# Performance work log

Measured on AMD Instinct MI355X. Metric: run time of the kernel, lower is better.

## Reference

```python
import jax, jax.numpy as jnp
import numpy as np

N, E, IN, HID, OUT, L = 50000, 800000, 128, 64, 40, 3


def setup_inputs() -> dict:
    key = jax.random.key(0)
    ks = jax.random.split(key, 10)
    x = jax.random.normal(ks[0], (N, IN), jnp.float32)
    edge_index = jax.random.randint(ks[1], (2, E), 0, N, dtype=jnp.int32)

    def u(k, shape, fan_in):
        s = 1.0 / np.sqrt(fan_in)
        return jax.random.uniform(k, shape, jnp.float32, -s, s)

    return {
        "x": x,
        "edge_index": edge_index,
        # former1 (NWGformerF): in -> hidden projection
        "Wf": u(ks[2], (IN, HID), IN),
        "bf": jnp.zeros((HID,), jnp.float32),
        # stacked GCNConv weights (hidden->hidden)
        "conv_W": u(ks[3], (L, HID, HID), HID),
        "conv_b": jnp.zeros((L, HID), jnp.float32),
        # residual linears
        "lin_W": u(ks[4], (L, HID, HID), HID),
        "lin_b": u(ks[5], (L, HID), HID),
        # batchnorm (eval mode: affine with running stats)
        "gamma": jnp.ones((L, HID), jnp.float32),
        "beta": jnp.zeros((L, HID), jnp.float32),
        "run_mean": jnp.zeros((L, HID), jnp.float32),
        "run_var": jnp.ones((L, HID), jnp.float32),
        # output head
        "pred_W": u(ks[6], (HID, OUT), HID),
        "pred_b": jnp.zeros((OUT,), jnp.float32),
    }


def reference(x, edge_index, Wf, bf, conv_W, conv_b, lin_W, lin_b,
              gamma, beta, run_mean, run_var, pred_W, pred_b):
    n = x.shape[0]
    src, dst = edge_index[0], edge_index[1]
    eps = 1e-5

    # GCN symmetric normalization with self-loops: deg over dst (+1 self loop)
    deg = jax.ops.segment_sum(jnp.ones(src.shape[0], x.dtype), dst,
                              num_segments=n) + 1.0
    dinv = jax.lax.rsqrt(deg)                      # [N]
    edge_coef = dinv[src] * dinv[dst]              # [E]
    self_coef = (dinv * dinv)[:, None]             # [N,1]

    def gcn(h, W, b):
        hw = h @ W                                 # [N,HID]
        agg = jax.ops.segment_sum(hw[src] * edge_coef[:, None], dst,
                                  num_segments=n)
        return agg + hw * self_coef + b

    # former1: in -> hidden (dropout is identity in eval mode)
    h = x @ Wf + bf

    for i in range(L):
        h = gcn(h, conv_W[i], conv_b[i]) + h @ lin_W[i] + lin_b[i]  # res
        h = (h - run_mean[i]) * (gamma[i] * jax.lax.rsqrt(run_var[i] + eps)) + beta[i]
        h = jax.nn.relu(h)

    return h @ pred_W + pred_b
```

## Files before the change

### kernel.cpp

```cpp
#include <hip/hip_runtime.h>
#include <hip/hip_bf16.h>
#include <hip/hip_fp16.h>

#define IN_DIM 128
#define HID 64
#define OUT_DIM 40
#define SPAD 68
#define CHUNKS 128

typedef __hip_bfloat16 bf16;
typedef unsigned short u16;
typedef _Float16 f16;
typedef __attribute__((ext_vector_type(8))) _Float16 f16x8;
typedef __attribute__((ext_vector_type(4))) float f32x4;

__device__ __forceinline__ float b2f(bf16 v) { return __bfloat162float(v); }
__device__ __forceinline__ float relu_f(float x) { return 0.5f * (x + fabsf(x)); }
__device__ __forceinline__ float ldv(const void* p, int i, int is32) {
    return is32 ? ((const float*)p)[i] : b2f(((const bf16*)p)[i]);
}

__global__ void MPNNs_60198261620971_kernel() {}

__global__ void canary_k(float* out, int m) {
    int i = blockIdx.x * blockDim.x + threadIdx.x;
    if (i < m) out[i] = 1234.0f;
}


__global__ __launch_bounds__(256) void hist_k(const int* __restrict__ dst,
                                              unsigned int* __restrict__ cnt,
                                              u16* __restrict__ rank,
                                              int e, int n, int n2, int chunk,
                                              const unsigned int* __restrict__ rv,
                                              int* __restrict__ flag) {
    __shared__ unsigned int hc[16384];
    if (blockIdx.x == 0 && threadIdx.x == 0)
        flag[0] = (rv[0] == 0x3F800000u) ? 1 : 0;
    int c = blockIdx.x >> 1, hf = blockIdx.x & 1;
    int w0 = hf << 14;
    int w1 = min(n2, w0 + 16384);
    int nw = w1 - w0;
    if (nw <= 0) return;
    for (int i = threadIdx.x; i < nw; i += 256) hc[i] = 0;
    __syncthreads();
    int e0 = c * chunk, e1 = min(e, e0 + chunk);
    for (int i = e0 + threadIdx.x; i < e1; i += 256) {
        int d = dst[i];
        if ((unsigned)d < (unsigned)n) {
            int w = d >> 1;
            if (w >= w0 && w < w1) {
                int sh = (d & 1) * 16;
                unsigned old = atomicAdd(&hc[w - w0], 1u << sh);
                rank[i] = (u16)((old >> sh) & 0xFFFFu);
            }
        }
    }
    __syncthreads();
    for (int i = threadIdx.x; i < nw; i += 256)
        cnt[(size_t)c * n2 + w0 + i] = hc[i];
}

__global__ __launch_bounds__(256) void former_k(const void* __restrict__ x,
                                                const void* __restrict__ Wf,
                                                const void* __restrict__ bfv,
                                                const int* __restrict__ dflag,
                                                float* __restrict__ h, int n) {
    __shared__ __align__(16) f16 wT[HID][IN_DIM + 8];
    int is32 = dflag[0];
    for (int i = threadIdx.x; i < IN_DIM * HID; i += 256) {
        int k = i >> 6, nn = i & 63;
        wT[nn][k] = (f16)ldv(Wf, i, is32);
    }
    __syncthreads();
    int wave = threadIdx.x >> 6, lane = threadIdx.x & 63;
    int m = lane & 15, quad = lane >> 4;
    int row0 = blockIdx.x * 64 + wave * 16;
    if (row0 >= n) return;
    int ar = row0 + m;
    int arc = (ar < n) ? ar : (n - 1);
    f16x8 a[4];
    if (is32) {
        const float* xp = (const float*)x + (size_t)arc * IN_DIM;
        #pragma unroll
        for (int cn = 0; cn < 4; cn++) {
            float4 u0 = *(const float4*)(xp + cn * 32 + quad * 8);
            float4 u1 = *(const float4*)(xp + cn * 32 + quad * 8 + 4);
            a[cn] = (f16x8){ (f16)u0.x, (f16)u0.y, (f16)u0.z, (f16)u0.w,
                             (f16)u1.x, (f16)u1.y, (f16)u1.z, (f16)u1.w };
        }
    } else {
        const bf16* xp = (const bf16*)x + (size_t)arc * IN_DIM;
        #pragma unroll
        for (int cn = 0; cn < 4; cn++)
            #pragma unroll
            for (int j = 0; j < 8; j++) a[cn][j] = (f16)b2f(xp[cn * 32 + quad * 8 + j]);
    }
    f32x4 acc[4];
    #pragma unroll
    for (int ct = 0; ct < 4; ct++) acc[ct] = (f32x4){0.f, 0.f, 0.f, 0.f};
    #pragma unroll
    for (int ct = 0; ct < 4; ct++) {
        int nn = ct * 16 + m;
        #pragma unroll
        for (int cn = 0; cn < 4; cn++) {
            f16x8 b = *(const f16x8*)&wT[nn][cn * 32 + quad * 8];
            acc[ct] = __builtin_amdgcn_mfma_f32_16x16x32_f16(a[cn], b, acc[ct], 0, 0, 0);
        }
    }
    float bias[4];
    #pragma unroll
    for (int ct = 0; ct < 4; ct++) bias[ct] = ldv(bfv, ct * 16 + m, is32);
    #pragma unroll
    for (int r = 0; r < 4; r++) {
        int row = row0 + quad * 4 + r;
        if (row < n) {
            #pragma unroll
            for (int ct = 0; ct < 4; ct++)
                h[(size_t)row * HID + ct * 16 + m] = acc[ct][r] + bias[ct];
        }
    }
}

__global__ void scan1B_k(unsigned int* __restrict__ cnt, int* __restrict__ row_ptr,
                         int* __restrict__ psum, float* __restrict__ dinv,
                         int n, int n2) {
    __shared__ unsigned int tot[512];
    __shared__ int sdata[1024];
    int tid = threadIdx.x;
    int w = blockIdx.x * 512 + tid;
    if (tid < 512) {
        unsigned acc = 0;
        if (w < n2) {
            size_t idx = w;
            for (int b = 0; b < CHUNKS; b += 8) {
                unsigned ww[8];
                #pragma unroll
                for (int j = 0; j < 8; j++) ww[j] = cnt[idx + (size_t)(b + j) * n2];
                #pragma unroll
                for (int j = 0; j < 8; j++) {
                    cnt[idx + (size_t)(b + j) * n2] = acc;
                    acc += ww[j];
                }
            }
        }
        tot[tid] = acc;
    }
    __syncthreads();
    int i = blockIdx.x * 1024 + tid;
    int v = 0;
    if (i < n) {
        v = (int)((tot[tid >> 1] >> ((tid & 1) * 16)) & 0xFFFFu);
        dinv[i] = rsqrtf((float)v + 1.0f);
    }
    sdata[tid] = v;
    __syncthreads();
    for (int off = 1; off < 1024; off <<= 1) {
        int t = (tid >= off) ? sdata[tid - off] : 0;
        __syncthreads();
        sdata[tid] += t;
        __syncthreads();
    }
    if (i < n) row_ptr[i] = sdata[tid] - v;
    if (tid == 1023) psum[blockIdx.x] = sdata[1023];
}

__global__ void scan2_k(int* __restrict__ psum, int* __restrict__ row_ptr, int nb, int n) {
    __shared__ int sdata[1024];
    int v = (threadIdx.x < nb) ? psum[threadIdx.x] : 0;
    sdata[threadIdx.x] = v;
    __syncthreads();
    for (int off = 1; off < 1024; off <<= 1) {
        int t = (threadIdx.x >= off) ? sdata[threadIdx.x - off] : 0;
        __syncthreads();
        sdata[threadIdx.x] += t;
        __syncthreads();
    }
    if (threadIdx.x < nb) psum[threadIdx.x] = sdata[threadIdx.x] - v;
    if (threadIdx.x == 1023) row_ptr[n] = sdata[1023];
}

__global__ void scan3_k(int* __restrict__ row_ptr, const int* __restrict__ psum, int n) {
    int i = blockIdx.x * blockDim.x + threadIdx.x;
    if (i < n) row_ptr[i] += psum[i >> 10];
}

__global__ __launch_bounds__(256) void filldense_k(const int* __restrict__ src,
                                                   const int* __restrict__ dst,
                                                   const int* __restrict__ row_ptr,
                                                   const unsigned int* __restrict__ cnt,
                                                   const u16* __restrict__ rank,
                                                   u16* __restrict__ col,
                                                   int e, int n, int n2, int chunk,
                                                   float* __restrict__ h,
                                                   const void* __restrict__ convW,
                                                   const void* __restrict__ linW,
                                                   const void* __restrict__ convB,
                                                   const void* __restrict__ linB,
                                                   const int* __restrict__ dflag,
                                                   const float* __restrict__ dinv,
                                                   __half* __restrict__ hws) {
    __shared__ __align__(16) f16 wT2[2][HID][72];
    if (blockIdx.x < CHUNKS) {
        int b = blockIdx.x;
        int e0 = b * chunk, e1 = min(e, e0 + chunk);
        for (int i = e0 + threadIdx.x; i < e1; i += 256) {
            int d = dst[i];
            if ((unsigned)d < (unsigned)n) {
                unsigned bw = cnt[(size_t)b * n2 + (d >> 1)];
                int base = (int)((bw >> ((d & 1) * 16)) & 0xFFFFu);
                col[row_ptr[d] + base + (int)rank[i]] = (u16)src[i];
            }
        }
        return;
    }
    int is32 = dflag[0];
    for (int i = threadIdx.x; i < HID * HID; i += 256) {
        int k = i >> 6, nn = i & 63;
        wT2[0][nn][k] = (f16)ldv(convW, i, is32);
        wT2[1][nn][k] = (f16)ldv(linW, i, is32);
    }
    __syncthreads();
    int wave = threadIdx.x >> 6, lane = threadIdx.x & 63;
    int m = lane & 15, quad = lane >> 4;
    int row0 = (int)(blockIdx.x - CHUNKS) * 64 + wave * 16;
    if (row0 >= n) return;
    int ar = row0 + m;
    const float* hp = h + (size_t)((ar < n) ? ar : 0) * HID;
    float4 v0 = *(const float4*)(hp + quad * 8);
    float4 v1 = *(const float4*)(hp + quad * 8 + 4);
    float4 v2 = *(const float4*)(hp + 32 + quad * 8);
    float4 v3 = *(const float4*)(hp + 32 + quad * 8 + 4);
    f16x8 a0 = { (f16)v0.x, (f16)v0.y, (f16)v0.z, (f16)v0.w,
                 (f16)v1.x, (f16)v1.y, (f16)v1.z, (f16)v1.w };
    f16x8 a1 = { (f16)v2.x, (f16)v2.y, (f16)v2.z, (f16)v2.w,
                 (f16)v3.x, (f16)v3.y, (f16)v3.z, (f16)v3.w };
    f32x4 acc[2][4];
    #pragma unroll
    for (int t = 0; t < 2; t++)
        #pragma unroll
        for (int ct = 0; ct < 4; ct++) acc[t][ct] = (f32x4){0.f, 0.f, 0.f, 0.f};
    #pragma unroll
    for (int ct = 0; ct < 4; ct++) {
        int nn = ct * 16 + m;
        f16x8 b00 = *(const f16x8*)&wT2[0][nn][quad * 8];
        f16x8 b01 = *(const f16x8*)&wT2[0][nn][32 + quad * 8];
        f16x8 b10 = *(const f16x8*)&wT2[1][nn][quad * 8];
        f16x8 b11 = *(const f16x8*)&wT2[1][nn][32 + quad * 8];
        acc[0][ct] = __builtin_amdgcn_mfma_f32_16x16x32_f16(a0, b00, acc[0][ct], 0, 0, 0);
        acc[0][ct] = __builtin_amdgcn_mfma_f32_16x16x32_f16(a1, b01, acc[0][ct], 0, 0, 0);
        acc[1][ct] = __builtin_amdgcn_mfma_f32_16x16x32_f16(a0, b10, acc[1][ct], 0, 0, 0);
        acc[1][ct] = __builtin_amdgcn_mfma_f32_16x16x32_f16(a1, b11, acc[1][ct], 0, 0, 0);
    }
    float cbv[4];
    #pragma unroll
    for (int ct = 0; ct < 4; ct++)
        cbv[ct] = ldv(convB, ct * 16 + m, is32) + ldv(linB, ct * 16 + m, is32);
    #pragma unroll
    for (int r = 0; r < 4; r++) {
        int row = row0 + quad * 4 + r;
        if (row < n) {
            float dv = dinv[row];
            #pragma unroll
            for (int ct = 0; ct < 4; ct++) {
                int colx = ct * 16 + m;
                hws[(size_t)row * HID + colx] = __float2half(acc[0][ct][r] * dv);
                h[(size_t)row * HID + colx] = acc[1][ct][r] + cbv[ct];
            }
        }
    }
}

__global__ __launch_bounds__(256) void dense_k(float* __restrict__ h,
                                               const void* __restrict__ convW,
                                               const void* __restrict__ linW,
                                               const void* __restrict__ convB,
                                               const void* __restrict__ linB,
                                               const int* __restrict__ dflag,
                                               const float* __restrict__ dinv,
                                               __half* __restrict__ hws, int n, int l) {
    __shared__ __align__(16) f16 wT2[2][HID][72];
    int is32 = dflag[0];
    int wOff = l * HID * HID, vOff = l * HID;
    for (int i = threadIdx.x; i < HID * HID; i += 256) {
        int k = i >> 6, nn = i & 63;
        wT2[0][nn][k] = (f16)ldv(convW, wOff + i, is32);
        wT2[1][nn][k] = (f16)ldv(linW, wOff + i, is32);
    }
    __syncthreads();
    int wave = threadIdx.x >> 6, lane = threadIdx.x & 63;
    int m = lane & 15, quad = lane >> 4;
    int row0 = blockIdx.x * 64 + wave * 16;
    if (row0 >= n) return;
    int ar = row0 + m;
    const float* hp = h + (size_t)((ar < n) ? ar : 0) * HID;
    float4 v0 = *(const float4*)(hp + quad * 8);
    float4 v1 = *(const float4*)(hp + quad * 8 + 4);
    float4 v2 = *(const float4*)(hp + 32 + quad * 8);
    float4 v3 = *(const float4*)(hp + 32 + quad * 8 + 4);
    f16x8 a0 = { (f16)v0.x, (f16)v0.y, (f16)v0.z, (f16)v0.w,
                 (f16)v1.x, (f16)v1.y, (f16)v1.z, (f16)v1.w };
    f16x8 a1 = { (f16)v2.x, (f16)v2.y, (f16)v2.z, (f16)v2.w,
                 (f16)v3.x, (f16)v3.y, (f16)v3.z, (f16)v3.w };
    f32x4 acc[2][4];
    #pragma unroll
    for (int t = 0; t < 2; t++)
        #pragma unroll
        for (int ct = 0; ct < 4; ct++) acc[t][ct] = (f32x4){0.f, 0.f, 0.f, 0.f};
    #pragma unroll
    for (int ct = 0; ct < 4; ct++) {
        int nn = ct * 16 + m;
        f16x8 b00 = *(const f16x8*)&wT2[0][nn][quad * 8];
        f16x8 b01 = *(const f16x8*)&wT2[0][nn][32 + quad * 8];
        f16x8 b10 = *(const f16x8*)&wT2[1][nn][quad * 8];
        f16x8 b11 = *(const f16x8*)&wT2[1][nn][32 + quad * 8];
        acc[0][ct] = __builtin_amdgcn_mfma_f32_16x16x32_f16(a0, b00, acc[0][ct], 0, 0, 0);
        acc[0][ct] = __builtin_amdgcn_mfma_f32_16x16x32_f16(a1, b01, acc[0][ct], 0, 0, 0);
        acc[1][ct] = __builtin_amdgcn_mfma_f32_16x16x32_f16(a0, b10, acc[1][ct], 0, 0, 0);
        acc[1][ct] = __builtin_amdgcn_mfma_f32_16x16x32_f16(a1, b11, acc[1][ct], 0, 0, 0);
    }
    float cbv[4];
    #pragma unroll
    for (int ct = 0; ct < 4; ct++)
        cbv[ct] = ldv(convB, vOff + ct * 16 + m, is32) + ldv(linB, vOff + ct * 16 + m, is32);
    #pragma unroll
    for (int r = 0; r < 4; r++) {
        int row = row0 + quad * 4 + r;
        if (row < n) {
            float dv = dinv[row];
            #pragma unroll
            for (int ct = 0; ct < 4; ct++) {
                int colx = ct * 16 + m;
                hws[(size_t)row * HID + colx] = __float2half(acc[0][ct][r] * dv);
                h[(size_t)row * HID + colx] = acc[1][ct][r] + cbv[ct];
            }
        }
    }
}

__global__ __launch_bounds__(256) void agg_k(const __half* __restrict__ hws,
                                             const float* __restrict__ dinv,
                                             const int* __restrict__ row_ptr,
                                             const u16* __restrict__ col,
                                             const void* __restrict__ gamma,
                                             const void* __restrict__ beta,
                                             const void* __restrict__ mean,
                                             const void* __restrict__ var,
                                             const int* __restrict__ dflag,
                                             float* __restrict__ h, int n, int l) {
    int gwave = (blockIdx.x * blockDim.x + threadIdx.x) >> 6;
    int lane = threadIdx.x & 63;
    int nw = (gridDim.x * blockDim.x) >> 6;
    int half = lane >> 5, c = lane & 31;
    const __half2* hws2 = (const __half2*)hws;
    int is32 = dflag[0];
    int vOff = l * HID;
    float mn0 = ldv(mean, vOff + 2 * c, is32),     mn1 = ldv(mean, vOff + 2 * c + 1, is32);
    float sc0 = ldv(gamma, vOff + 2 * c, is32) * rsqrtf(ldv(var, vOff + 2 * c, is32) + 1e-5f);
    float sc1 = ldv(gamma, vOff + 2 * c + 1, is32) * rsqrtf(ldv(var, vOff + 2 * c + 1, is32) + 1e-5f);
    float bt0 = ldv(beta, vOff + 2 * c, is32),     bt1 = ldv(beta, vOff + 2 * c + 1, is32);
    for (int v = gwave; v < n; v += nw) {
        int s0 = row_ptr[v], s1 = row_ptr[v + 1];
        float2 a[8];
        #pragma unroll
        for (int g = 0; g < 8; g++) a[g] = make_float2(0.f, 0.f);
        if (half == 0) {
            float2 s = __half22float2(hws2[(size_t)v * 32 + c]);
            a[0].x += s.x; a[0].y += s.y;
        }
        for (int j0 = s0; j0 < s1; j0 += 64) {
            int myidx = (j0 + lane < s1) ? (int)col[j0 + lane] : 0;
            int cnt = min(64, s1 - j0);
            int t = 0;
            for (; t + 16 <= cnt; t += 16) {
                #pragma unroll
                for (int g = 0; g < 8; g++) {
                    int idx = __shfl(myidx, t + 2 * g + half);
                    idx = ((unsigned)idx < (unsigned)n) ? idx : 0;
                    float2 p = __half22float2(hws2[(size_t)idx * 32 + c]);
                    a[g].x += p.x; a[g].y += p.y;
                }
            }
            for (; t < cnt; t += 2) {
                int has = (t + half) < cnt;
                int sel = t + half; if (sel >= cnt) sel = cnt - 1;
                int idx = __shfl(myidx, sel);
                idx = ((unsigned)idx < (unsigned)n) ? idx : 0;
                float2 p = __half22float2(hws2[(size_t)idx * 32 + c]);
                if (has) { a[0].x += p.x; a[0].y += p.y; }
            }
        }
        float ax = ((a[0].x + a[1].x) + (a[2].x + a[3].x)) + ((a[4].x + a[5].x) + (a[6].x + a[7].x));
        float ay = ((a[0].y + a[1].y) + (a[2].y + a[3].y)) + ((a[4].y + a[5].y) + (a[6].y + a[7].y));
        float px = __shfl(ax, c + 32);
        float py = __shfl(ay, c + 32);
        if (half == 0) {
            float dv = dinv[v];
            float2 basev = *(const float2*)&h[(size_t)v * HID + 2 * c];
            float vx = dv * (ax + px) + basev.x;
            float vy = dv * (ay + py) + basev.y;
            vx = (vx - mn0) * sc0 + bt0;
            vy = (vy - mn1) * sc1 + bt1;
            float2 o = make_float2(relu_f(vx), relu_f(vy));
            *(float2*)&h[(size_t)v * HID + 2 * c] = o;
        }
    }
}

__global__ __launch_bounds__(256) void pred_k(const float* __restrict__ h,
                                              const void* __restrict__ pW,
                                              const void* __restrict__ pb,
                                              const int* __restrict__ dflag,
                                              void* __restrict__ out, int n) {
    __shared__ float sW[HID * OUT_DIM];
    __shared__ float sh[64 * SPAD];
    int is32 = dflag[0];
    if (is32) {
        const float4* w4 = (const float4*)pW;
        for (int i = threadIdx.x; i < HID * OUT_DIM / 4; i += 256) ((float4*)sW)[i] = w4[i];
    } else {
        for (int i = threadIdx.x; i < HID * OUT_DIM; i += 256) sW[i] = b2f(((const bf16*)pW)[i]);
    }
    int tid = threadIdx.x, cg = tid & 15, rg = tid >> 4;
    int rowBase = blockIdx.x * 64;
    #pragma unroll
    for (int pass = 0; pass < 4; pass++) {
        int r = pass * 16 + (tid >> 4);
        int c = (tid & 15) * 4;
        int gr = rowBase + r;
        float4 v = (gr < n) ? *(const float4*)&h[(size_t)gr * HID + c] : make_float4(0.f, 0.f, 0.f, 0.f);
        *(float4*)&sh[r * SPAD + c] = v;
    }
    __syncthreads();
    if (cg < 10) {
        float acc[4][4];
        #pragma unroll
        for (int i = 0; i < 4; i++)
            #pragma unroll
            for (int j = 0; j < 4; j++) acc[i][j] = 0.f;
        for (int k = 0; k < 64; k += 4) {
            float4 hr[4], w[4];
            #pragma unroll
            for (int i = 0; i < 4; i++) hr[i] = *(float4*)&sh[(rg * 4 + i) * SPAD + k];
            #pragma unroll
            for (int j = 0; j < 4; j++) w[j] = *(float4*)&sW[(k + j) * OUT_DIM + cg * 4];
            #pragma unroll
            for (int i = 0; i < 4; i++) {
                const float* hh = (const float*)&hr[i];
                #pragma unroll
                for (int j = 0; j < 4; j++) {
                    const float* ww = (const float*)&w[j];
                    acc[i][0] += hh[j] * ww[0];
                    acc[i][1] += hh[j] * ww[1];
                    acc[i][2] += hh[j] * ww[2];
                    acc[i][3] += hh[j] * ww[3];
                }
            }
        }
        float b0 = ldv(pb, cg * 4 + 0, is32), b1 = ldv(pb, cg * 4 + 1, is32);
        float b2 = ldv(pb, cg * 4 + 2, is32), b3 = ldv(pb, cg * 4 + 3, is32);
        #pragma unroll
        for (int i = 0; i < 4; i++) {
            int r = rowBase + rg * 4 + i;
            if (r < n) {
                if (is32) {
                    float4 o = make_float4(acc[i][0] + b0, acc[i][1] + b1, acc[i][2] + b2, acc[i][3] + b3);
                    *(float4*)((float*)out + (size_t)r * OUT_DIM + cg * 4) = o;
                } else {
                    bf16* ob = (bf16*)out + (size_t)r * OUT_DIM + cg * 4;
                    ob[0] = __float2bfloat16(acc[i][0] + b0);
                    ob[1] = __float2bfloat16(acc[i][1] + b1);
                    ob[2] = __float2bfloat16(acc[i][2] + b2);
                    ob[3] = __float2bfloat16(acc[i][3] + b3);
                }
            }
        }
    }
}


extern "C" void kernel_launch(void* const* d_in, const int* in_sizes, int n_in,
                              void* d_out, int out_size, void* d_ws, size_t ws_size,
                              hipStream_t stream) {
    const void* x     = d_in[0];
    const int*  ei    = (const int*)d_in[1];
    const void* Wf    = d_in[2];
    const void* bfv   = d_in[3];
    const void* convW = d_in[4];
    const void* convB = d_in[5];
    const void* linW  = d_in[6];
    const void* linB  = d_in[7];
    const void* gamma = d_in[8];
    const void* beta  = d_in[9];
    const void* rmean = d_in[10];
    const void* rvar  = d_in[11];
    const void* pW    = d_in[12];
    const void* pb    = d_in[13];

    const int n = in_sizes[0] / IN_DIM;
    const int e = in_sizes[1] / 2;
    const int L = in_sizes[5] / HID;
    const int n2 = (n + 1) / 2;

    const int* src = ei;
    const int* dst = ei + e;

    char* ws = (char*)d_ws;
    size_t off = 0;
    auto take = [&](size_t bytes) {
        char* p = ws + off;
        off = (off + bytes + 255) & ~(size_t)255;
        return p;
    };
    float*        h       = (float*)take((size_t)n * HID * 4);
    __half*       hws     = (__half*)take((size_t)n * HID * 2);
    float*        dinv    = (float*)take((size_t)n * 4);
    unsigned int* cnt     = (unsigned int*)take((size_t)CHUNKS * n2 * 4);
    int*          row_ptr = (int*)take((size_t)(n + 1) * 4);
    u16*          rank    = (u16*)take((size_t)e * 2);
    u16*          colbuf  = (u16*)take((size_t)e * 2);
    int*          psum    = (int*)take(1024 * 4);
    int*          dflag   = (int*)take(256);

    if (off > ws_size || n > 65535) {
        canary_k<<<(out_size + 255) / 256, 256, 0, stream>>>((float*)d_out, out_size);
        return;
    }

    const int nblocks = (n + 255) / 256;
    const int nb1024  = (n + 1023) / 1024;
    const int nb64    = (n + 63) / 64;
    const int chunk   = (((e + CHUNKS - 1) / CHUNKS) + 255) & ~255;

    hist_k<<<2 * CHUNKS, 256, 0, stream>>>(dst, cnt, rank, e, n, n2, chunk,
                                           (const unsigned int*)rvar, dflag);
    former_k<<<nb64, 256, 0, stream>>>(x, Wf, bfv, dflag, h, n);
    scan1B_k<<<nb1024, 1024, 0, stream>>>(cnt, row_ptr, psum, dinv, n, n2);
    scan2_k<<<1, 1024, 0, stream>>>(psum, row_ptr, nb1024, n);
    scan3_k<<<nblocks, 256, 0, stream>>>(row_ptr, psum, n);
    filldense_k<<<CHUNKS + nb64, 256, 0, stream>>>(src, dst, row_ptr, cnt, rank, colbuf,
                                                   e, n, n2, chunk, h, convW, linW,
                                                   convB, linB, dflag, dinv, hws);
    for (int l = 0; l < L; l++) {
        if (l > 0)
            dense_k<<<nb64, 256, 0, stream>>>(h, convW, linW, convB, linB,
                                              dflag, dinv, hws, n, l);
        agg_k<<<2048, 256, 0, stream>>>(hws, dinv, row_ptr, colbuf,
                                        gamma, beta, rmean, rvar, dflag, h, n, l);
    }

    pred_k<<<nb64, 256, 0, stream>>>(h, pW, pb, dflag, (void*)d_out, n);
}
```

Before: 306.8 us.

## Fuse former, scans, CSR fill, and GCN layers into one cooperative kernel

Replaces the former projection, the scan2/scan3 prefix-sum passes, the CSR fill, and the per-layer dense and aggregation kernels with a single persistent cooperative kernel that uses grid.sync between phases. The final scan uses wave shuffles instead of a 1024-thread block. The aim is to remove roughly ten kernel launches and their gaps. In exchange the grid is limited to the number of blocks that can be co-resident, grid-wide barriers are added, and launch bounds may constrain registers.

```diff
diff --git a/kernel.cpp b/kernel.cpp
--- a/kernel.cpp
+++ b/kernel.cpp
@@ -1,12 +1,15 @@
 #include <hip/hip_runtime.h>
 #include <hip/hip_bf16.h>
 #include <hip/hip_fp16.h>
+#include <hip/hip_cooperative_groups.h>
 
 #define IN_DIM 128
 #define HID 64
 #define OUT_DIM 40
 #define SPAD 68
 #define CHUNKS 128
+
+namespace cg = cooperative_groups;
 
 typedef __hip_bfloat16 bf16;
 typedef unsigned short u16;
@@ -61,67 +64,6 @@
         cnt[(size_t)c * n2 + w0 + i] = hc[i];
 }
 
-__global__ __launch_bounds__(256) void former_k(const void* __restrict__ x,
-                                                const void* __restrict__ Wf,
-                                                const void* __restrict__ bfv,
-                                                const int* __restrict__ dflag,
-                                                float* __restrict__ h, int n) {
-    __shared__ __align__(16) f16 wT[HID][IN_DIM + 8];
-    int is32 = dflag[0];
-    for (int i = threadIdx.x; i < IN_DIM * HID; i += 256) {
-        int k = i >> 6, nn = i & 63;
-        wT[nn][k] = (f16)ldv(Wf, i, is32);
-    }
-    __syncthreads();
-    int wave = threadIdx.x >> 6, lane = threadIdx.x & 63;
-    int m = lane & 15, quad = lane >> 4;
-    int row0 = blockIdx.x * 64 + wave * 16;
-    if (row0 >= n) return;
-    int ar = row0 + m;
-    int arc = (ar < n) ? ar : (n - 1);
-    f16x8 a[4];
-    if (is32) {
-        const float* xp = (const float*)x + (size_t)arc * IN_DIM;
-        #pragma unroll
-        for (int cn = 0; cn < 4; cn++) {
-            float4 u0 = *(const float4*)(xp + cn * 32 + quad * 8);
-            float4 u1 = *(const float4*)(xp + cn * 32 + quad * 8 + 4);
-            a[cn] = (f16x8){ (f16)u0.x, (f16)u0.y, (f16)u0.z, (f16)u0.w,
-                             (f16)u1.x, (f16)u1.y, (f16)u1.z, (f16)u1.w };
-        }
-    } else {
-        const bf16* xp = (const bf16*)x + (size_t)arc * IN_DIM;
-        #pragma unroll
-        for (int cn = 0; cn < 4; cn++)
-            #pragma unroll
-            for (int j = 0; j < 8; j++) a[cn][j] = (f16)b2f(xp[cn * 32 + quad * 8 + j]);
-    }
-    f32x4 acc[4];
-    #pragma unroll
-    for (int ct = 0; ct < 4; ct++) acc[ct] = (f32x4){0.f, 0.f, 0.f, 0.f};
-    #pragma unroll
-    for (int ct = 0; ct < 4; ct++) {
-        int nn = ct * 16 + m;
-        #pragma unroll
-        for (int cn = 0; cn < 4; cn++) {
-            f16x8 b = *(const f16x8*)&wT[nn][cn * 32 + quad * 8];
-            acc[ct] = __builtin_amdgcn_mfma_f32_16x16x32_f16(a[cn], b, acc[ct], 0, 0, 0);
-        }
-    }
-    float bias[4];
-    #pragma unroll
-    for (int ct = 0; ct < 4; ct++) bias[ct] = ldv(bfv, ct * 16 + m, is32);
-    #pragma unroll
-    for (int r = 0; r < 4; r++) {
-        int row = row0 + quad * 4 + r;
-        if (row < n) {
-            #pragma unroll
-            for (int ct = 0; ct < 4; ct++)
-                h[(size_t)row * HID + ct * 16 + m] = acc[ct][r] + bias[ct];
-        }
-    }
-}
-
 __global__ void scan1B_k(unsigned int* __restrict__ cnt, int* __restrict__ row_ptr,
                          int* __restrict__ psum, float* __restrict__ dinv,
                          int n, int n2) {
@@ -165,245 +107,231 @@
     if (tid == 1023) psum[blockIdx.x] = sdata[1023];
 }
 
-__global__ void scan2_k(int* __restrict__ psum, int* __restrict__ row_ptr, int nb, int n) {
-    __shared__ int sdata[1024];
-    int v = (threadIdx.x < nb) ? psum[threadIdx.x] : 0;
-    sdata[threadIdx.x] = v;
-    __syncthreads();
-    for (int off = 1; off < 1024; off <<= 1) {
-        int t = (threadIdx.x >= off) ? sdata[threadIdx.x - off] : 0;
+
+struct MegaP {
+    const int* src; const int* dst;
+    const unsigned int* cnt; const u16* rank;
+    int* row_ptr; int* psum; u16* col;
+    const float* dinv; float* h; __half* hws;
+    const void* x; const void* Wf; const void* bfv;
+    const void* convW; const void* linW; const void* convB; const void* linB;
+    const void* gamma; const void* beta; const void* mean; const void* var;
+    const int* dflag;
+    int e, n, n2, chunk, nb1024, nb64, L;
+};
+
+__global__ __launch_bounds__(256, 4) void mega_k(MegaP p) {
+    cg::grid_group grid = cg::this_grid();
+    __shared__ __align__(16) f16 wU[2][HID][72];
+    int tid = threadIdx.x, bid = blockIdx.x, nblk = gridDim.x;
+    int is32 = p.dflag[0];
+    int wave = tid >> 6, lane = tid & 63;
+    int m = lane & 15, quad = lane >> 4;
+
+    if (bid == nblk - 1 && wave == 0) {
+        int nb = p.nb1024;
+        int v0 = (lane < nb) ? p.psum[lane] : 0;
+        int v = v0;
+        #pragma unroll
+        for (int off = 1; off < 64; off <<= 1) {
+            int u = __shfl_up(v, off);
+            if (lane >= off) v += u;
+        }
+        if (lane < nb) p.psum[lane] = v - v0;
+        if (lane == nb - 1) p.row_ptr[p.n] = v;
+    }
+    {
+        f16 (*wT)[IN_DIM + 8] = (f16(*)[IN_DIM + 8])wU;
+        for (int i = tid; i < IN_DIM * HID; i += 256) {
+            int k = i >> 6, nn = i & 63;
+            wT[nn][k] = (f16)ldv(p.Wf, i, is32);
+        }
         __syncthreads();
-        sdata[threadIdx.x] += t;
-        __syncthreads();
-    }
-    if (threadIdx.x < nb) psum[threadIdx.x] = sdata[threadIdx.x] - v;
-    if (threadIdx.x == 1023) row_ptr[n] = sdata[1023];
-}
-
-__global__ void scan3_k(int* __restrict__ row_ptr, const int* __restrict__ psum, int n) {
-    int i = blockIdx.x * blockDim.x + threadIdx.x;
-    if (i < n) row_ptr[i] += psum[i >> 10];
-}
-
-__global__ __launch_bounds__(256) void filldense_k(const int* __restrict__ src,
-                                                   const int* __restrict__ dst,
-                                                   const int* __restrict__ row_ptr,
-                                                   const unsigned int* __restrict__ cnt,
-                                                   const u16* __restrict__ rank,
-                                                   u16* __restrict__ col,
-                                                   int e, int n, int n2, int chunk,
-                                                   float* __restrict__ h,
-                                                   const void* __restrict__ convW,
-                                                   const void* __restrict__ linW,
-                                                   const void* __restrict__ convB,
-                                                   const void* __restrict__ linB,
-                                                   const int* __restrict__ dflag,
-                                                   const float* __restrict__ dinv,
-                                                   __half* __restrict__ hws) {
-    __shared__ __align__(16) f16 wT2[2][HID][72];
-    if (blockIdx.x < CHUNKS) {
-        int b = blockIdx.x;
-        int e0 = b * chunk, e1 = min(e, e0 + chunk);
-        for (int i = e0 + threadIdx.x; i < e1; i += 256) {
-            int d = dst[i];
-            if ((unsigned)d < (unsigned)n) {
-                unsigned bw = cnt[(size_t)b * n2 + (d >> 1)];
-                int base = (int)((bw >> ((d & 1) * 16)) & 0xFFFFu);
-                col[row_ptr[d] + base + (int)rank[i]] = (u16)src[i];
-            }
-        }
-        return;
-    }
-    int is32 = dflag[0];
-    for (int i = threadIdx.x; i < HID * HID; i += 256) {
-        int k = i >> 6, nn = i & 63;
-        wT2[0][nn][k] = (f16)ldv(convW, i, is32);
-        wT2[1][nn][k] = (f16)ldv(linW, i, is32);
-    }
-    __syncthreads();
-    int wave = threadIdx.x >> 6, lane = threadIdx.x & 63;
-    int m = lane & 15, quad = lane >> 4;
-    int row0 = (int)(blockIdx.x - CHUNKS) * 64 + wave * 16;
-    if (row0 >= n) return;
-    int ar = row0 + m;
-    const float* hp = h + (size_t)((ar < n) ? ar : 0) * HID;
-    float4 v0 = *(const float4*)(hp + quad * 8);
-    float4 v1 = *(const float4*)(hp + quad * 8 + 4);
-    float4 v2 = *(const float4*)(hp + 32 + quad * 8);
-    float4 v3 = *(const float4*)(hp + 32 + quad * 8 + 4);
-    f16x8 a0 = { (f16)v0.x, (f16)v0.y, (f16)v0.z, (f16)v0.w,
-                 (f16)v1.x, (f16)v1.y, (f16)v1.z, (f16)v1.w };
-    f16x8 a1 = { (f16)v2.x, (f16)v2.y, (f16)v2.z, (f16)v2.w,
-                 (f16)v3.x, (f16)v3.y, (f16)v3.z, (f16)v3.w };
-    f32x4 acc[2][4];
-    #pragma unroll
-    for (int t = 0; t < 2; t++)
+        float bias[4];
         #pragma unroll
-        for (int ct = 0; ct < 4; ct++) acc[t][ct] = (f32x4){0.f, 0.f, 0.f, 0.f};
-    #pragma unroll
-    for (int ct = 0; ct < 4; ct++) {
-        int nn = ct * 16 + m;
-        f16x8 b00 = *(const f16x8*)&wT2[0][nn][quad * 8];
-        f16x8 b01 = *(const f16x8*)&wT2[0][nn][32 + quad * 8];
-        f16x8 b10 = *(const f16x8*)&wT2[1][nn][quad * 8];
-        f16x8 b11 = *(const f16x8*)&wT2[1][nn][32 + quad * 8];
-        acc[0][ct] = __builtin_amdgcn_mfma_f32_16x16x32_f16(a0, b00, acc[0][ct], 0, 0, 0);
-        acc[0][ct] = __builtin_amdgcn_mfma_f32_16x16x32_f16(a1, b01, acc[0][ct], 0, 0, 0);
-        acc[1][ct] = __builtin_amdgcn_mfma_f32_16x16x32_f16(a0, b10, acc[1][ct], 0, 0, 0);
-        acc[1][ct] = __builtin_amdgcn_mfma_f32_16x16x32_f16(a1, b11, acc[1][ct], 0, 0, 0);
-    }
-    float cbv[4];
-    #pragma unroll
-    for (int ct = 0; ct < 4; ct++)
-        cbv[ct] = ldv(convB, ct * 16 + m, is32) + ldv(linB, ct * 16 + m, is32);
-    #pragma unroll
-    for (int r = 0; r < 4; r++) {
-        int row = row0 + quad * 4 + r;
-        if (row < n) {
-            float dv = dinv[row];
+        for (int ct = 0; ct < 4; ct++) bias[ct] = ldv(p.bfv, ct * 16 + m, is32);
+        for (int tile = bid; tile < p.nb64; tile += nblk) {
+            int row0 = tile * 64 + wave * 16;
+            if (row0 >= p.n) continue;
+            int ar = row0 + m;
+            int arc = (ar < p.n) ? ar : (p.n - 1);
+            f16x8 a[4];
+            if (is32) {
+                const float* xp = (const float*)p.x + (size_t)arc * IN_DIM;
+                #pragma unroll
+                for (int cn = 0; cn < 4; cn++) {
+                    float4 u0 = *(const float4*)(xp + cn * 32 + quad * 8);
+                    float4 u1 = *(const float4*)(xp + cn * 32 + quad * 8 + 4);
+                    a[cn] = (f16x8){ (f16)u0.x, (f16)u0.y, (f16)u0.z, (f16)u0.w,
+                                     (f16)u1.x, (f16)u1.y, (f16)u1.z, (f16)u1.w };
+                }
+            } else {
+                const bf16* xp = (const bf16*)p.x + (size_t)arc * IN_DIM;
+                #pragma unroll
+                for (int cn = 0; cn < 4; cn++)
+                    #pragma unroll
+                    for (int j = 0; j < 8; j++) a[cn][j] = (f16)b2f(xp[cn * 32 + quad * 8 + j]);
+            }
+            f32x4 acc[4];
+            #pragma unroll
+            for (int ct = 0; ct < 4; ct++) acc[ct] = (f32x4){0.f, 0.f, 0.f, 0.f};
             #pragma unroll
             for (int ct = 0; ct < 4; ct++) {
-                int colx = ct * 16 + m;
-                hws[(size_t)row * HID + colx] = __float2half(acc[0][ct][r] * dv);
-                h[(size_t)row * HID + colx] = acc[1][ct][r] + cbv[ct];
-            }
-        }
-    }
-}
-
-__global__ __launch_bounds__(256) void dense_k(float* __restrict__ h,
-                                               const void* __restrict__ convW,
-                                               const void* __restrict__ linW,
-                                               const void* __restrict__ convB,
-                                               const void* __restrict__ linB,
-                                               const int* __restrict__ dflag,
-                                               const float* __restrict__ dinv,
-                                               __half* __restrict__ hws, int n, int l) {
-    __shared__ __align__(16) f16 wT2[2][HID][72];
-    int is32 = dflag[0];
-    int wOff = l * HID * HID, vOff = l * HID;
-    for (int i = threadIdx.x; i < HID * HID; i += 256) {
-        int k = i >> 6, nn = i & 63;
-        wT2[0][nn][k] = (f16)ldv(convW, wOff + i, is32);
-        wT2[1][nn][k] = (f16)ldv(linW, wOff + i, is32);
-    }
-    __syncthreads();
-    int wave = threadIdx.x >> 6, lane = threadIdx.x & 63;
-    int m = lane & 15, quad = lane >> 4;
-    int row0 = blockIdx.x * 64 + wave * 16;
-    if (row0 >= n) return;
-    int ar = row0 + m;
-    const float* hp = h + (size_t)((ar < n) ? ar : 0) * HID;
-    float4 v0 = *(const float4*)(hp + quad * 8);
-    float4 v1 = *(const float4*)(hp + quad * 8 + 4);
-    float4 v2 = *(const float4*)(hp + 32 + quad * 8);
-    float4 v3 = *(const float4*)(hp + 32 + quad * 8 + 4);
-    f16x8 a0 = { (f16)v0.x, (f16)v0.y, (f16)v0.z, (f16)v0.w,
-                 (f16)v1.x, (f16)v1.y, (f16)v1.z, (f16)v1.w };
-    f16x8 a1 = { (f16)v2.x, (f16)v2.y, (f16)v2.z, (f16)v2.w,
-                 (f16)v3.x, (f16)v3.y, (f16)v3.z, (f16)v3.w };
-    f32x4 acc[2][4];
-    #pragma unroll
-    for (int t = 0; t < 2; t++)
-        #pragma unroll
-        for (int ct = 0; ct < 4; ct++) acc[t][ct] = (f32x4){0.f, 0.f, 0.f, 0.f};
-    #pragma unroll
-    for (int ct = 0; ct < 4; ct++) {
-        int nn = ct * 16 + m;
-        f16x8 b00 = *(const f16x8*)&wT2[0][nn][quad * 8];
-        f16x8 b01 = *(const f16x8*)&wT2[0][nn][32 + quad * 8];
-        f16x8 b10 = *(const f16x8*)&wT2[1][nn][quad * 8];
-        f16x8 b11 = *(const f16x8*)&wT2[1][nn][32 + quad * 8];
-        acc[0][ct] = __builtin_amdgcn_mfma_f32_16x16x32_f16(a0, b00, acc[0][ct], 0, 0, 0);
-        acc[0][ct] = __builtin_amdgcn_mfma_f32_16x16x32_f16(a1, b01, acc[0][ct], 0, 0, 0);
-        acc[1][ct] = __builtin_amdgcn_mfma_f32_16x16x32_f16(a0, b10, acc[1][ct], 0, 0, 0);
-        acc[1][ct] = __builtin_amdgcn_mfma_f32_16x16x32_f16(a1, b11, acc[1][ct], 0, 0, 0);
-    }
-    float cbv[4];
-    #pragma unroll
-    for (int ct = 0; ct < 4; ct++)
-        cbv[ct] = ldv(convB, vOff + ct * 16 + m, is32) + ldv(linB, vOff + ct * 16 + m, is32);
-    #pragma unroll
-    for (int r = 0; r < 4; r++) {
-        int row = row0 + quad * 4 + r;
-        if (row < n) {
-            float dv = dinv[row];
-            #pragma unroll
-            for (int ct = 0; ct < 4; ct++) {
-                int colx = ct * 16 + m;
-                hws[(size_t)row * HID + colx] = __float2half(acc[0][ct][r] * dv);
-                h[(size_t)row * HID + colx] = acc[1][ct][r] + cbv[ct];
-            }
-        }
-    }
-}
-
-__global__ __launch_bounds__(256) void agg_k(const __half* __restrict__ hws,
-                                             const float* __restrict__ dinv,
-                                             const int* __restrict__ row_ptr,
-                                             const u16* __restrict__ col,
-                                             const void* __restrict__ gamma,
-                                             const void* __restrict__ beta,
-                                             const void* __restrict__ mean,
-                                             const void* __restrict__ var,
-                                             const int* __restrict__ dflag,
-                                             float* __restrict__ h, int n, int l) {
-    int gwave = (blockIdx.x * blockDim.x + threadIdx.x) >> 6;
-    int lane = threadIdx.x & 63;
-    int nw = (gridDim.x * blockDim.x) >> 6;
-    int half = lane >> 5, c = lane & 31;
-    const __half2* hws2 = (const __half2*)hws;
-    int is32 = dflag[0];
-    int vOff = l * HID;
-    float mn0 = ldv(mean, vOff + 2 * c, is32),     mn1 = ldv(mean, vOff + 2 * c + 1, is32);
-    float sc0 = ldv(gamma, vOff + 2 * c, is32) * rsqrtf(ldv(var, vOff + 2 * c, is32) + 1e-5f);
-    float sc1 = ldv(gamma, vOff + 2 * c + 1, is32) * rsqrtf(ldv(var, vOff + 2 * c + 1, is32) + 1e-5f);
-    float bt0 = ldv(beta, vOff + 2 * c, is32),     bt1 = ldv(beta, vOff + 2 * c + 1, is32);
-    for (int v = gwave; v < n; v += nw) {
-        int s0 = row_ptr[v], s1 = row_ptr[v + 1];
-        float2 a[8];
-        #pragma unroll
-        for (int g = 0; g < 8; g++) a[g] = make_float2(0.f, 0.f);
-        if (half == 0) {
-            float2 s = __half22float2(hws2[(size_t)v * 32 + c]);
-            a[0].x += s.x; a[0].y += s.y;
-        }
-        for (int j0 = s0; j0 < s1; j0 += 64) {
-            int myidx = (j0 + lane < s1) ? (int)col[j0 + lane] : 0;
-            int cnt = min(64, s1 - j0);
-            int t = 0;
-            for (; t + 16 <= cnt; t += 16) {
-                #pragma unroll
-                for (int g = 0; g < 8; g++) {
-                    int idx = __shfl(myidx, t + 2 * g + half);
-                    idx = ((unsigned)idx < (unsigned)n) ? idx : 0;
-                    float2 p = __half22float2(hws2[(size_t)idx * 32 + c]);
-                    a[g].x += p.x; a[g].y += p.y;
-                }
-            }
-            for (; t < cnt; t += 2) {
-                int has = (t + half) < cnt;
-                int sel = t + half; if (sel >= cnt) sel = cnt - 1;
-                int idx = __shfl(myidx, sel);
-                idx = ((unsigned)idx < (unsigned)n) ? idx : 0;
-                float2 p = __half22float2(hws2[(size_t)idx * 32 + c]);
-                if (has) { a[0].x += p.x; a[0].y += p.y; }
-            }
-        }
-        float ax = ((a[0].x + a[1].x) + (a[2].x + a[3].x)) + ((a[4].x + a[5].x) + (a[6].x + a[7].x));
-        float ay = ((a[0].y + a[1].y) + (a[2].y + a[3].y)) + ((a[4].y + a[5].y) + (a[6].y + a[7].y));
-        float px = __shfl(ax, c + 32);
-        float py = __shfl(ay, c + 32);
-        if (half == 0) {
-            float dv = dinv[v];
-            float2 basev = *(const float2*)&h[(size_t)v * HID + 2 * c];
-            float vx = dv * (ax + px) + basev.x;
-            float vy = dv * (ay + py) + basev.y;
-            vx = (vx - mn0) * sc0 + bt0;
-            vy = (vy - mn1) * sc1 + bt1;
-            float2 o = make_float2(relu_f(vx), relu_f(vy));
-            *(float2*)&h[(size_t)v * HID + 2 * c] = o;
-        }
+                int nn = ct * 16 + m;
+                #pragma unroll
+                for (int cn = 0; cn < 4; cn++) {
+                    f16x8 b = *(const f16x8*)&wT[nn][cn * 32 + quad * 8];
+                    acc[ct] = __builtin_amdgcn_mfma_f32_16x16x32_f16(a[cn], b, acc[ct], 0, 0, 0);
+                }
+            }
+            #pragma unroll
+            for (int r = 0; r < 4; r++) {
+                int row = row0 + quad * 4 + r;
+                if (row < p.n) {
+                    #pragma unroll
+                    for (int ct = 0; ct < 4; ct++)
+                        p.h[(size_t)row * HID + ct * 16 + m] = acc[ct][r] + bias[ct];
+                }
+            }
+        }
+    }
+    grid.sync();
+
+    for (int i = bid * 256 + tid; i < p.n; i += nblk * 256)
+        p.row_ptr[i] += p.psum[i >> 10];
+    grid.sync();
+
+    for (int l = 0; l < p.L; l++) {
+        if (l == 0 && bid < CHUNKS) {
+            int e0 = bid * p.chunk, e1 = min(p.e, e0 + p.chunk);
+            for (int i = e0 + tid; i < e1; i += 256) {
+                int d = p.dst[i];
+                if ((unsigned)d < (unsigned)p.n) {
+                    unsigned bw = p.cnt[(size_t)bid * p.n2 + (d >> 1)];
+                    int base = (int)((bw >> ((d & 1) * 16)) & 0xFFFFu);
+                    p.col[p.row_ptr[d] + base + (int)p.rank[i]] = (u16)p.src[i];
+                }
+            }
+        } else {
+            int tstart = (l == 0) ? bid - CHUNKS : bid;
+            int tstride = (l == 0) ? nblk - CHUNKS : nblk;
+            int wOff = l * HID * HID, vOff = l * HID;
+            for (int i = tid; i < HID * HID; i += 256) {
+                int k = i >> 6, nn = i & 63;
+                wU[0][nn][k] = (f16)ldv(p.convW, wOff + i, is32);
+                wU[1][nn][k] = (f16)ldv(p.linW, wOff + i, is32);
+            }
+            __syncthreads();
+            float cbv[4];
+            #pragma unroll
+            for (int ct = 0; ct < 4; ct++)
+                cbv[ct] = ldv(p.convB, vOff + ct * 16 + m, is32)
+                        + ldv(p.linB, vOff + ct * 16 + m, is32);
+            for (int tile = tstart; tile < p.nb64; tile += tstride) {
+                int row0 = tile * 64 + wave * 16;
+                if (row0 >= p.n) continue;
+                int ar = row0 + m;
+                const float* hp = p.h + (size_t)((ar < p.n) ? ar : 0) * HID;
+                float4 v0 = *(const float4*)(hp + quad * 8);
+                float4 v1 = *(const float4*)(hp + quad * 8 + 4);
+                float4 v2 = *(const float4*)(hp + 32 + quad * 8);
+                float4 v3 = *(const float4*)(hp + 32 + quad * 8 + 4);
+                f16x8 a0 = { (f16)v0.x, (f16)v0.y, (f16)v0.z, (f16)v0.w,
+                             (f16)v1.x, (f16)v1.y, (f16)v1.z, (f16)v1.w };
+                f16x8 a1 = { (f16)v2.x, (f16)v2.y, (f16)v2.z, (f16)v2.w,
+                             (f16)v3.x, (f16)v3.y, (f16)v3.z, (f16)v3.w };
+                f32x4 acc[2][4];
+                #pragma unroll
+                for (int t = 0; t < 2; t++)
+                    #pragma unroll
+                    for (int ct = 0; ct < 4; ct++) acc[t][ct] = (f32x4){0.f, 0.f, 0.f, 0.f};
+                #pragma unroll
+                for (int ct = 0; ct < 4; ct++) {
+                    int nn = ct * 16 + m;
+                    f16x8 b00 = *(const f16x8*)&wU[0][nn][quad * 8];
+                    f16x8 b01 = *(const f16x8*)&wU[0][nn][32 + quad * 8];
+                    f16x8 b10 = *(const f16x8*)&wU[1][nn][quad * 8];
+                    f16x8 b11 = *(const f16x8*)&wU[1][nn][32 + quad * 8];
+                    acc[0][ct] = __builtin_amdgcn_mfma_f32_16x16x32_f16(a0, b00, acc[0][ct], 0, 0, 0);
+                    acc[0][ct] = __builtin_amdgcn_mfma_f32_16x16x32_f16(a1, b01, acc[0][ct], 0, 0, 0);
+                    acc[1][ct] = __builtin_amdgcn_mfma_f32_16x16x32_f16(a0, b10, acc[1][ct], 0, 0, 0);
+                    acc[1][ct] = __builtin_amdgcn_mfma_f32_16x16x32_f16(a1, b11, acc[1][ct], 0, 0, 0);
+                }
+                #pragma unroll
+                for (int r = 0; r < 4; r++) {
+                    int row = row0 + quad * 4 + r;
+                    if (row < p.n) {
+                        float dv = p.dinv[row];
+                        #pragma unroll
+                        for (int ct = 0; ct < 4; ct++) {
+                            int colx = ct * 16 + m;
+                            p.hws[(size_t)row * HID + colx] = __float2half(acc[0][ct][r] * dv);
+                            p.h[(size_t)row * HID + colx] = acc[1][ct][r] + cbv[ct];
+                        }
+                    }
+                }
+            }
+        }
+        grid.sync();
+
+        {
+            int gwave = (bid * 256 + tid) >> 6;
+            int nw = (nblk * 256) >> 6;
+            int half = lane >> 5, c = lane & 31;
+            const __half2* hws2 = (const __half2*)p.hws;
+            int vOff = l * HID;
+            float mn0 = ldv(p.mean, vOff + 2 * c, is32), mn1 = ldv(p.mean, vOff + 2 * c + 1, is32);
+            float sc0 = ldv(p.gamma, vOff + 2 * c, is32) * rsqrtf(ldv(p.var, vOff + 2 * c, is32) + 1e-5f);
+            float sc1 = ldv(p.gamma, vOff + 2 * c + 1, is32) * rsqrtf(ldv(p.var, vOff + 2 * c + 1, is32) + 1e-5f);
+            float bt0 = ldv(p.beta, vOff + 2 * c, is32), bt1 = ldv(p.beta, vOff + 2 * c + 1, is32);
+            for (int v = gwave; v < p.n; v += nw) {
+                int s0 = p.row_ptr[v], s1 = p.row_ptr[v + 1];
+                float2 a[8];
+                #pragma unroll
+                for (int g = 0; g < 8; g++) a[g] = make_float2(0.f, 0.f);
+                if (half == 0) {
+                    float2 s = __half22float2(hws2[(size_t)v * 32 + c]);
+                    a[0].x += s.x; a[0].y += s.y;
+                }
+                for (int j0 = s0; j0 < s1; j0 += 64) {
+                    int myidx = (j0 + lane < s1) ? (int)p.col[j0 + lane] : 0;
+                    int cnt2 = min(64, s1 - j0);
+                    int t = 0;
+                    for (; t + 16 <= cnt2; t += 16) {
+                        #pragma unroll
+                        for (int g = 0; g < 8; g++) {
+                            int idx = __shfl(myidx, t + 2 * g + half);
+                            idx = ((unsigned)idx < (unsigned)p.n) ? idx : 0;
+                            float2 q = __half22float2(hws2[(size_t)idx * 32 + c]);
+                            a[g].x += q.x; a[g].y += q.y;
+                        }
+                    }
+                    for (; t < cnt2; t += 2) {
+                        int has = (t + half) < cnt2;
+                        int sel = t + half; if (sel >= cnt2) sel = cnt2 - 1;
+                        int idx = __shfl(myidx, sel);
+                        idx = ((unsigned)idx < (unsigned)p.n) ? idx : 0;
+                        float2 q = __half22float2(hws2[(size_t)idx * 32 + c]);
+                        if (has) { a[0].x += q.x; a[0].y += q.y; }
+                    }
+                }
+                float ax = ((a[0].x + a[1].x) + (a[2].x + a[3].x)) + ((a[4].x + a[5].x) + (a[6].x + a[7].x));
+                float ay = ((a[0].y + a[1].y) + (a[2].y + a[3].y)) + ((a[4].y + a[5].y) + (a[6].y + a[7].y));
+                float px = __shfl(ax, c + 32);
+                float py = __shfl(ay, c + 32);
+                if (half == 0) {
+                    float dv = p.dinv[v];
+                    float2 basev = *(const float2*)&p.h[(size_t)v * HID + 2 * c];
+                    float vx = dv * (ax + px) + basev.x;
+                    float vy = dv * (ay + py) + basev.y;
+                    vx = (vx - mn0) * sc0 + bt0;
+                    vy = (vy - mn1) * sc1 + bt1;
+                    float2 o = make_float2(relu_f(vx), relu_f(vy));
+                    *(float2*)&p.h[(size_t)v * HID + 2 * c] = o;
+                }
+            }
+        }
+        grid.sync();
     }
 }
 
@@ -421,7 +349,7 @@
     } else {
         for (int i = threadIdx.x; i < HID * OUT_DIM; i += 256) sW[i] = b2f(((const bf16*)pW)[i]);
     }
-    int tid = threadIdx.x, cg = tid & 15, rg = tid >> 4;
+    int tid = threadIdx.x, cg2 = tid & 15, rg = tid >> 4;
     int rowBase = blockIdx.x * 64;
     #pragma unroll
     for (int pass = 0; pass < 4; pass++) {
@@ -432,7 +360,7 @@
         *(float4*)&sh[r * SPAD + c] = v;
     }
     __syncthreads();
-    if (cg < 10) {
+    if (cg2 < 10) {
         float acc[4][4];
         #pragma unroll
         for (int i = 0; i < 4; i++)
@@ -443,7 +371,7 @@
             #pragma unroll
             for (int i = 0; i < 4; i++) hr[i] = *(float4*)&sh[(rg * 4 + i) * SPAD + k];
             #pragma unroll
-            for (int j = 0; j < 4; j++) w[j] = *(float4*)&sW[(k + j) * OUT_DIM + cg * 4];
+            for (int j = 0; j < 4; j++) w[j] = *(float4*)&sW[(k + j) * OUT_DIM + cg2 * 4];
             #pragma unroll
             for (int i = 0; i < 4; i++) {
                 const float* hh = (const float*)&hr[i];
@@ -457,17 +385,17 @@
                 }
             }
         }
-        float b0 = ldv(pb, cg * 4 + 0, is32), b1 = ldv(pb, cg * 4 + 1, is32);
-        float b2 = ldv(pb, cg * 4 + 2, is32), b3 = ldv(pb, cg * 4 + 3, is32);
+        float b0 = ldv(pb, cg2 * 4 + 0, is32), b1 = ldv(pb, cg2 * 4 + 1, is32);
+        float b2 = ldv(pb, cg2 * 4 + 2, is32), b3 = ldv(pb, cg2 * 4 + 3, is32);
         #pragma unroll
         for (int i = 0; i < 4; i++) {
             int r = rowBase + rg * 4 + i;
             if (r < n) {
                 if (is32) {
                     float4 o = make_float4(acc[i][0] + b0, acc[i][1] + b1, acc[i][2] + b2, acc[i][3] + b3);
-                    *(float4*)((float*)out + (size_t)r * OUT_DIM + cg * 4) = o;
+                    *(float4*)((float*)out + (size_t)r * OUT_DIM + cg2 * 4) = o;
                 } else {
-                    bf16* ob = (bf16*)out + (size_t)r * OUT_DIM + cg * 4;
+                    bf16* ob = (bf16*)out + (size_t)r * OUT_DIM + cg2 * 4;
                     ob[0] = __float2bfloat16(acc[i][0] + b0);
                     ob[1] = __float2bfloat16(acc[i][1] + b1);
                     ob[2] = __float2bfloat16(acc[i][2] + b2);
@@ -527,27 +455,40 @@
         return;
     }
 
-    const int nblocks = (n + 255) / 256;
-    const int nb1024  = (n + 1023) / 1024;
-    const int nb64    = (n + 63) / 64;
-    const int chunk   = (((e + CHUNKS - 1) / CHUNKS) + 255) & ~255;
+    const int nb1024 = (n + 1023) / 1024;
+    const int nb64   = (n + 63) / 64;
+    const int chunk  = (((e + CHUNKS - 1) / CHUNKS) + 255) & ~255;
+
+    int devBlk = 0;
+    if (hipOccupancyMaxActiveBlocksPerMultiprocessor(&devBlk, (const void*)mega_k, 256, 0)
+        != hipSuccess || devBlk < 1) devBlk = 2;
+    int dev = 0; hipGetDevice(&dev);
+    int numCU = 0;
+    if (hipDeviceGetAttribute(&numCU, hipDeviceAttributeMultiprocessorCount, dev)
+        != hipSuccess || numCU < 1) numCU = 256;
+    int grid = devBlk * numCU;
+    if (grid > 2048) grid = 2048;
+    if (grid < CHUNKS + 2) {
+        canary_k<<<(out_size + 255) / 256, 256, 0, stream>>>((float*)d_out, out_size);
+        return;
+    }
 
     hist_k<<<2 * CHUNKS, 256, 0, stream>>>(dst, cnt, rank, e, n, n2, chunk,
                                            (const unsigned int*)rvar, dflag);
-    former_k<<<nb64, 256, 0, stream>>>(x, Wf, bfv, dflag, h, n);
     scan1B_k<<<nb1024, 1024, 0, stream>>>(cnt, row_ptr, psum, dinv, n, n2);
-    scan2_k<<<1, 1024, 0, stream>>>(psum, row_ptr, nb1024, n);
-    scan3_k<<<nblocks, 256, 0, stream>>>(row_ptr, psum, n);
-    filldense_k<<<CHUNKS + nb64, 256, 0, stream>>>(src, dst, row_ptr, cnt, rank, colbuf,
-                                                   e, n, n2, chunk, h, convW, linW,
-                                                   convB, linB, dflag, dinv, hws);
-    for (int l = 0; l < L; l++) {
-        if (l > 0)
-            dense_k<<<nb64, 256, 0, stream>>>(h, convW, linW, convB, linB,
-                                              dflag, dinv, hws, n, l);
-        agg_k<<<2048, 256, 0, stream>>>(hws, dinv, row_ptr, colbuf,
-                                        gamma, beta, rmean, rvar, dflag, h, n, l);
-    }
+
+    MegaP mp;
+    mp.src = src; mp.dst = dst; mp.cnt = cnt; mp.rank = rank;
+    mp.row_ptr = row_ptr; mp.psum = psum; mp.col = colbuf;
+    mp.dinv = dinv; mp.h = h; mp.hws = hws;
+    mp.x = x; mp.Wf = Wf; mp.bfv = bfv;
+    mp.convW = convW; mp.linW = linW; mp.convB = convB; mp.linB = linB;
+    mp.gamma = gamma; mp.beta = beta; mp.mean = rmean; mp.var = rvar;
+    mp.dflag = dflag;
+    mp.e = e; mp.n = n; mp.n2 = n2; mp.chunk = chunk;
+    mp.nb1024 = nb1024; mp.nb64 = nb64; mp.L = L;
+    void* args[] = { (void*)&mp };
+    hipLaunchCooperativeKernel((const void*)mega_k, dim3(grid), dim3(256), args, 0, stream);
 
     pred_k<<<nb64, 256, 0, stream>>>(h, pW, pb, dflag, (void*)d_out, n);
 }
```

Measured after the change: 936.5 us. +205.2%, slower.
